# Optimization experiments

Hardware: AMD Instinct MI355X
Metric: run time of the kernel (lower is better)

Reference implementation:

```python
import jax, jax.numpy as jnp
import numpy as np

NUM_TOKENS = 14
DIM = 128
B, N = 8, 128
NUM_ROUNDS = 5


def setup_inputs() -> dict:
    key = jax.random.key(0)
    ks = jax.random.split(key, 10)
    s = 1.0 / np.sqrt(DIM)
    return {
        "tok": jax.random.randint(ks[0], (B, N), 0, NUM_TOKENS),
        "A": jax.random.uniform(ks[1], (B, N, N), dtype=jnp.float32),
        "embed": jax.random.normal(ks[2], (NUM_TOKENS, DIM), dtype=jnp.float32),
        "W1": jax.random.normal(ks[3], (DIM, 2 * DIM), dtype=jnp.float32) * s,
        "b1": jax.random.normal(ks[4], (DIM,), dtype=jnp.float32) * s,
        "W2": jax.random.normal(ks[5], (DIM, DIM), dtype=jnp.float32) * s,
        "b2": jax.random.normal(ks[6], (DIM,), dtype=jnp.float32) * s,
        "Wo1": jax.random.normal(ks[7], (DIM, DIM), dtype=jnp.float32) * s,
        "bo1": jax.random.normal(ks[8], (DIM,), dtype=jnp.float32) * s,
        "Wo2": jax.random.normal(ks[9], (10, DIM), dtype=jnp.float32) * s,
    }


def reference(tok, A, embed, W1, b1, W2, b2, Wo1, bo1, Wo2):
    # Dropout is identity (eval mode / inference reference).
    x = embed[tok]  # [B, N, D]
    d = x.shape[-1]
    # fc1 on concat(x_i, x_j) decomposes into two per-node projections:
    # fc1([x_i, x_j]) = x_i @ W1a^T + x_j @ W1b^T + b1
    W1a, W1b = W1[:, :d], W1[:, d:]
    A_t = jnp.swapaxes(A, 1, 2)  # A.transpose(1, 2)
    for _ in range(NUM_ROUNDS):
        hi = jnp.einsum("bnd,ed->bne", x, W1a)
        hj = jnp.einsum("bnd,ed->bne", x, W1b)
        # pairwise edge MLP: [B, N, N, D]
        h = jax.nn.relu(hi[:, :, None, :] + hj[:, None, :, :] + b1)
        m = jax.nn.relu(jnp.einsum("bijd,ed->bije", h, W2) + b2)
        # mask by transposed adjacency and sum over neighbors j (axis 2)
        msg = jnp.einsum("bij,bije->bie", A_t, m)
        x = x + msg
    def head(z):
        return jax.nn.relu(z @ Wo1.T + bo1) @ Wo2.T
    out = head(x[:, 0, :])                       # [B, 10]
    x_all = head(x.reshape(-1, d)).reshape(x.shape[0], x.shape[1], 10)
    return (out, x_all)
```

## Files before the change

kernel.cpp:

```cpp
#include <hip/hip_runtime.h>
#include <hip/hip_bf16.h>

#define NN 128
#define DD 128

typedef __attribute__((ext_vector_type(8))) short bf16x8;
typedef __attribute__((ext_vector_type(4))) float floatx4;
typedef __attribute__((ext_vector_type(2))) float floatx2;

__device__ __forceinline__ unsigned short f2bf(float f) {
    unsigned int bits = __float_as_uint(f);
    unsigned int r = bits + 0x7FFFu + ((bits >> 16) & 1u);
    return (unsigned short)(r >> 16);
}

__device__ __forceinline__ unsigned short f2bf_hw(float f) {
    unsigned int r;
    asm("v_cvt_pk_bf16_f32 %0, %1, %2" : "=v"(r) : "v"(f), "v"(f));
    return (unsigned short)r;
}

__device__ __forceinline__ unsigned int f2bf_pk(float lo, float hi) {
    unsigned int r;
    asm("v_cvt_pk_bf16_f32 %0, %1, %2" : "=v"(r) : "v"(lo), "v"(hi));
    return r;
}

#define WS_HJB0 0
#define WS_HJB1 65536
#define WS_W1T  131072
#define WS_W2B  148480
#define WS_TABA 157184
#define WS_TABB 158976
#define WS_CNT  159872

__global__ __launch_bounds__(256) void k_init(const int* __restrict__ tok,
                                              const float* __restrict__ embf,
                                              const float* __restrict__ W1f,
                                              const float* __restrict__ b1f,
                                              const float* __restrict__ W2f,
                                              float* __restrict__ ws) {
    unsigned short* gw1t = (unsigned short*)(ws + WS_W1T);
    unsigned short* gw2b = (unsigned short*)(ws + WS_W2B);
    float* taba = ws + WS_TABA;
    unsigned int* tabb32 = (unsigned int*)(ws + WS_TABB);
    int* cnt = (int*)(ws + WS_CNT);
    int blk = blockIdx.x, t = threadIdx.x;

    if (blk == 0) {
        __shared__ __align__(16) unsigned short wt[256 * 136];
        __shared__ __align__(16) unsigned short et_[16 * 136];
        __shared__ float b1s[128];
        for (int idx = t; idx < 256 * 136; idx += 256) {
            int e = idx / 136, d = idx - e * 136;
            wt[idx] = (d < 128) ? f2bf(W1f[(e & 127) * 256 + (e >> 7) * 128 + d])
                                : (unsigned short)0;
        }
        for (int i = t; i < 16 * 136; i += 256) et_[i] = 0;
        if (t < 128) b1s[t] = b1f[t];
        __syncthreads();
        if (t < 224) {
            int v = t >> 4, d0 = (t & 15) * 8;
#pragma unroll
            for (int k2 = 0; k2 < 8; ++k2) et_[v * 136 + d0 + k2] = f2bf(embf[v * 128 + d0 + k2]);
        }
        __syncthreads();
        int wv = t >> 6, lane = t & 63, col = lane & 15, quad = lane >> 4;
        bf16x8 af[4];
#pragma unroll
        for (int ks = 0; ks < 4; ++ks)
            af[ks] = *reinterpret_cast<const bf16x8*>(&et_[col * 136 + ks * 32 + quad * 8]);
#pragma unroll
        for (int c = 0; c < 4; ++c) {
            int nt = wv * 4 + c;
            floatx4 acc = (floatx4){0.f, 0.f, 0.f, 0.f};
#pragma unroll
            for (int ks = 0; ks < 4; ++ks)
                acc = __builtin_amdgcn_mfma_f32_16x16x32_bf16(af[ks],
                        *reinterpret_cast<const bf16x8*>(&wt[(nt * 16 + col) * 136 + ks * 32 + quad * 8]),
                        acc, 0, 0, 0);
            if (nt < 8) {
#pragma unroll
                for (int rr = 0; rr < 4; ++rr) {
                    int v = quad * 4 + rr;
                    if (v < 14) taba[v * 128 + nt * 16 + col] = acc[rr];
                }
            } else {
                int d = (nt - 8) * 16 + col;
                float bv = b1s[d];
#pragma unroll
                for (int rr = 0; rr < 4; ++rr) {
                    float val = acc[rr] + bv;
                    float po = __shfl_xor(val, 1, 64);
                    int v = quad * 4 + rr;
                    if (!(col & 1) && v < 14)
                        tabb32[v * 64 + (d >> 1)] =
                            (unsigned int)f2bf(val) | ((unsigned int)f2bf(po) << 16);
                }
            }
        }
    } else if (blk < 10) {
        int base = (blk - 1) * 4096;
#pragma unroll
        for (int it = 0; it < 16; ++it) {
            int idx = base + it * 256 + t;
            if (idx < 256 * 136) {
                int e = idx / 136, d = idx - e * 136;
                gw1t[idx] = (d < 128) ? f2bf(W1f[(e & 127) * 256 + (e >> 7) * 128 + d])
                                      : (unsigned short)0;
            }
        }
    } else if (blk < 15) {
        int base = (blk - 10) * 4096;
#pragma unroll
        for (int it = 0; it < 16; ++it) {
            int idx = base + it * 256 + t;
            if (idx < 128 * 136) {
                int e = idx / 136, d = idx - e * 136;
                gw2b[idx] = (d < 128) ? f2bf(W2f[e * 128 + d]) : (unsigned short)0;
            }
        }
    } else {
#pragma unroll
        for (int it = 0; it < 4; ++it) cnt[it * 256 + t] = 0;
    }
}

__global__ __launch_bounds__(512, 2) void k_main(const int* __restrict__ tokp,
                                                 const float* __restrict__ embf,
                                                 const float* __restrict__ Af,
                                                 const float* __restrict__ b1f,
                                                 const float* __restrict__ b2f,
                                                 const float* __restrict__ Wo1f,
                                                 const float* __restrict__ bo1f,
                                                 const float* __restrict__ Wo2f,
                                                 float* __restrict__ ws,
                                                 float* __restrict__ outp) {
    __shared__ __align__(16) unsigned short w1t[256 * 136];
    __shared__ __align__(16) unsigned short w2b[128 * 136];
    __shared__ __align__(16) unsigned short xo[4 * 136];
    __shared__ __align__(16) float red[4][4][128];
    __shared__ __align__(16) float zs[4][128];
    __shared__ float a_s[4][128];
    __shared__ __align__(16) float hja_s[4][128];

    const unsigned short* gw1t = (const unsigned short*)(ws + WS_W1T);
    const unsigned short* gw2b = (const unsigned short*)(ws + WS_W2B);
    const float* taba = ws + WS_TABA;
    const unsigned short* tabb16 = (const unsigned short*)(ws + WS_TABB);
    int* cnt = (int*)(ws + WS_CNT);

    int blk = blockIdx.x;
    int b = blk & 7, g = blk >> 3, i0 = g * 4;
    int t = threadIdx.x;
    int wave = t >> 6, lane = t & 63;
    int col = lane & 15, quad = lane >> 4;

    {
        const uint4* s1 = (const uint4*)gw1t; uint4* d1 = (uint4*)w1t;
#pragma unroll
        for (int it = 0; it < 9; ++it) { int idx = it * 512 + t; if (idx < 4352) d1[idx] = s1[idx]; }
        const uint4* s2 = (const uint4*)gw2b; uint4* d2 = (uint4*)w2b;
#pragma unroll
        for (int it = 0; it < 5; ++it) { int idx = it * 512 + t; if (idx < 2176) d2[idx] = s2[idx]; }
    }
    int we = wave & 1, wj = wave >> 1;
    int ebase = we * 64, jbase = wj * 32;
    float b1r0 = 0.f, b1r1 = 0.f;
    if (wave >= 4) {
        b1r0 = b1f[((wave - 4) * 2 + 0) * 16 + col];
        b1r1 = b1f[((wave - 4) * 2 + 1) * 16 + col];
    }
    float b2r[4];
#pragma unroll
    for (int et = 0; et < 4; ++et) b2r[et] = b2f[ebase + et * 16 + col];
    a_s[t >> 7][t & 127] = Af[(b * NN + (t & 127)) * NN + i0 + (t >> 7)];

    int ii_own = t >> 7, e_own = t & 127;
    int trow = tokp[b * NN + i0 + ii_own];
    float xown = embf[trow * DD + e_own];
    hja_s[ii_own][e_own] = taba[trow * 128 + e_own];
    __syncthreads();

    for (int r = 0; r < 5; ++r) {
        unsigned short* gbw = (unsigned short*)(ws + ((r & 1) ? WS_HJB1 : WS_HJB0));

        if (r > 0) {
            bf16x8 af[4];
#pragma unroll
            for (int ks = 0; ks < 4; ++ks) {
                bf16x8 z = {0, 0, 0, 0, 0, 0, 0, 0};
                af[ks] = (col < 4) ? *reinterpret_cast<const bf16x8*>(&xo[col * 136 + ks * 32 + quad * 8]) : z;
            }
            floatx4 acc[2];
            acc[0] = (floatx4){0.f, 0.f, 0.f, 0.f};
            acc[1] = (floatx4){0.f, 0.f, 0.f, 0.f};
#pragma unroll
            for (int u = 0; u < 2; ++u)
#pragma unroll
                for (int ks = 0; ks < 4; ++ks) {
                    int nt = wave * 2 + u;
                    acc[u] = __builtin_amdgcn_mfma_f32_16x16x32_bf16(af[ks],
                        *reinterpret_cast<const bf16x8*>(&w1t[(nt * 16 + col) * 136 + ks * 32 + quad * 8]),
                        acc[u], 0, 0, 0);
                }
            if (wave < 4) {
                if (quad == 0) {
#pragma unroll
                    for (int u = 0; u < 2; ++u)
#pragma unroll
                        for (int rr = 0; rr < 4; ++rr)
                            hja_s[rr][(wave * 2 + u) * 16 + col] = acc[u][rr];
                }
            } else {
#pragma unroll
                for (int u = 0; u < 2; ++u) {
                    float bv = u ? b1r1 : b1r0;
                    int d = ((wave - 4) * 2 + u) * 16 + col;
#pragma unroll
                    for (int rr = 0; rr < 4; ++rr) {
                        float val = acc[u][rr] + bv;
                        float po = __shfl_xor(val, 1, 64);
                        if (quad == 0 && !(col & 1)) {
                            int row = b * NN + i0 + rr;
                            __hip_atomic_store((unsigned int*)gbw + row * 64 + (d >> 1),
                                               f2bf_pk(val, po),
                                               __ATOMIC_RELAXED, __HIP_MEMORY_SCOPE_AGENT);
                        }
                    }
                }
            }
            __atomic_signal_fence(__ATOMIC_SEQ_CST);
            __builtin_amdgcn_s_waitcnt(0);
            __syncthreads();
            if (t == 0) {
                int* myc = cnt + (b * 4 + (r - 1)) * 32;
                __hip_atomic_fetch_add(myc, 1, __ATOMIC_RELAXED, __HIP_MEMORY_SCOPE_AGENT);
                while (__hip_atomic_load(myc, __ATOMIC_RELAXED, __HIP_MEMORY_SCOPE_AGENT) < 32)
                    __builtin_amdgcn_s_sleep(1);
            }
            __syncthreads();
        }

        union U4 { bf16x8 v; unsigned int u[4]; };
        U4 L[2][4];
        {
            const unsigned short* base0;
            const unsigned short* base1;
            if (r == 0) {
                base0 = tabb16 + (size_t)tokp[b * NN + jbase + col] * 128;
                base1 = tabb16 + (size_t)tokp[b * NN + jbase + 16 + col] * 128;
            } else {
                base0 = gbw + (size_t)(b * NN + jbase + col) * 128;
                base1 = gbw + (size_t)(b * NN + jbase + 16 + col) * 128;
            }
            base0 += quad * 8; base1 += quad * 8;
            asm volatile(
                "global_load_dwordx4 %0, %8, off sc0 sc1\n\t"
                "global_load_dwordx4 %1, %8, off offset:64 sc0 sc1\n\t"
                "global_load_dwordx4 %2, %8, off offset:128 sc0 sc1\n\t"
                "global_load_dwordx4 %3, %8, off offset:192 sc0 sc1\n\t"
                "global_load_dwordx4 %4, %9, off sc0 sc1\n\t"
                "global_load_dwordx4 %5, %9, off offset:64 sc0 sc1\n\t"
                "global_load_dwordx4 %6, %9, off offset:128 sc0 sc1\n\t"
                "global_load_dwordx4 %7, %9, off offset:192 sc0 sc1"
                : "=&v"(L[0][0].v), "=&v"(L[0][1].v), "=&v"(L[0][2].v), "=&v"(L[0][3].v),
                  "=&v"(L[1][0].v), "=&v"(L[1][1].v), "=&v"(L[1][2].v), "=&v"(L[1][3].v)
                : "v"(base0), "v"(base1)
                : "memory");
        }
        bf16x8 bw[4][4];
#pragma unroll
        for (int et = 0; et < 4; ++et)
#pragma unroll
            for (int ks = 0; ks < 4; ++ks)
                bw[et][ks] = *reinterpret_cast<const bf16x8*>(&w2b[(ebase + et * 16 + col) * 136 + ks * 32 + quad * 8]);
        asm volatile("s_waitcnt vmcnt(0)" ::: "memory");
        __builtin_amdgcn_sched_barrier(0);

        floatx2 hjc[2][4][4];
#pragma unroll
        for (int jt = 0; jt < 2; ++jt)
#pragma unroll
            for (int ks = 0; ks < 4; ++ks)
#pragma unroll
                for (int p = 0; p < 4; ++p) {
                    floatx2 h2;
                    h2.x = __uint_as_float(L[jt][ks].u[p] << 16);
                    h2.y = __uint_as_float(L[jt][ks].u[p] & 0xFFFF0000u);
                    hjc[jt][ks][p] = h2;
                }

#pragma unroll
        for (int ii = 0; ii < 4; ++ii) {
            floatx4 acc2[2][4];
#pragma unroll
            for (int jt = 0; jt < 2; ++jt)
#pragma unroll
                for (int et = 0; et < 4; ++et) acc2[jt][et] = (floatx4){0.f, 0.f, 0.f, 0.f};
#pragma unroll
            for (int ks = 0; ks < 4; ++ks) {
                int k0 = ks * 32 + quad * 8;
                floatx2 ha[4];
#pragma unroll
                for (int p = 0; p < 4; ++p)
                    ha[p] = *reinterpret_cast<const floatx2*>(&hja_s[ii][k0 + 2 * p]);
#pragma unroll
                for (int jt = 0; jt < 2; ++jt) {
                    U4 Ho;
#pragma unroll
                    for (int p = 0; p < 4; ++p) {
                        floatx2 s2;
                        asm("v_pk_add_f32 %0, %1, %2" : "=v"(s2) : "v"(hjc[jt][ks][p]), "v"(ha[p]));
                        float f0 = fmaxf(s2.x, 0.f);
                        float f1 = fmaxf(s2.y, 0.f);
                        Ho.u[p] = f2bf_pk(f0, f1);
                    }
#pragma unroll
                    for (int et = 0; et < 4; ++et)
                        acc2[jt][et] = __builtin_amdgcn_mfma_f32_16x16x32_bf16(Ho.v, bw[et][ks], acc2[jt][et], 0, 0, 0);
                }
            }
#pragma unroll
            for (int et = 0; et < 4; ++et) {
                float be = b2r[et];
                float s = 0.f;
#pragma unroll
                for (int jt = 0; jt < 2; ++jt) {
                    int j0 = jbase + jt * 16 + quad * 4;
#pragma unroll
                    for (int rr = 0; rr < 4; ++rr)
                        s += a_s[ii][j0 + rr] * fmaxf(acc2[jt][et][rr] + be, 0.f);
                }
                s += __shfl_xor(s, 16, 64);
                s += __shfl_xor(s, 32, 64);
                if (quad == 0) red[wj][ii][ebase + et * 16 + col] = s;
            }
        }
        __syncthreads();
        {
            float msg = red[0][ii_own][e_own] + red[1][ii_own][e_own]
                      + red[2][ii_own][e_own] + red[3][ii_own][e_own];
            xown += msg;
            if (r < 4) xo[ii_own * 136 + e_own] = f2bf_hw(xown);
            else       zs[ii_own][e_own] = xown;
        }
        if (r < 4) __syncthreads();
    }

    float* wo1s = (float*)w1t;
#pragma unroll
    for (int it = 0; it < 8; ++it) {
        int idx4 = it * 512 + t;
        int e = idx4 >> 5, d4 = idx4 & 31;
        float4 wv = reinterpret_cast<const float4*>(Wo1f)[idx4];
        *reinterpret_cast<float4*>(&wo1s[e * 136 + d4 * 4]) = wv;
    }
    __syncthreads();
    {
        int e = t & 127, ii = t >> 7;
        float acc = 0.f;
#pragma unroll
        for (int d4 = 0; d4 < 32; ++d4) {
            float4 w = *reinterpret_cast<const float4*>(&wo1s[e * 136 + d4 * 4]);
            float4 z = *reinterpret_cast<const float4*>(&zs[ii][d4 * 4]);
            acc += w.x * z.x + w.y * z.y + w.z * z.z + w.w * z.w;
        }
        ((float*)red)[ii * 128 + e] = fmaxf(acc + bo1f[e], 0.f);
    }
    __syncthreads();
    if (t < 40) {
        int ii = t / 10, o = t - ii * 10;
        const float* rsrow = (const float*)red + ii * 128;
        const float4* w2r = reinterpret_cast<const float4*>(Wo2f + o * DD);
        float s = 0.f;
#pragma unroll
        for (int e4 = 0; e4 < 32; ++e4) {
            float4 rv = *reinterpret_cast<const float4*>(&rsrow[e4 * 4]);
            float4 wv = w2r[e4];
            s += rv.x * wv.x + rv.y * wv.y + rv.z * wv.z + rv.w * wv.w;
        }
        int row = b * NN + i0 + ii;
        outp[80 + row * 10 + o] = s;
        if (i0 + ii == 0) outp[b * 10 + o] = s;
    }
}

extern "C" void kernel_launch(void* const* d_in, const int* in_sizes, int n_in,
                              void* d_out, int out_size, void* d_ws, size_t ws_size,
                              hipStream_t stream) {
    const int*   tok  = (const int*)d_in[0];
    const float* Af   = (const float*)d_in[1];
    const float* embf = (const float*)d_in[2];
    const float* W1f  = (const float*)d_in[3];
    const float* b1f  = (const float*)d_in[4];
    const float* W2f  = (const float*)d_in[5];
    const float* b2f  = (const float*)d_in[6];
    const float* Wo1f = (const float*)d_in[7];
    const float* bo1f = (const float*)d_in[8];
    const float* Wo2f = (const float*)d_in[9];

    float* ws  = (float*)d_ws;
    float* out = (float*)d_out;

    k_init<<<16, 256, 0, stream>>>(tok, embf, W1f, b1f, W2f, ws);
    k_main<<<256, 512, 0, stream>>>(tok, embf, Af, b1f, b2f, Wo1f, bo1f, Wo2f, ws, out);
}
```

Baseline: 172.2 us.

## Double block size to 1024 threads, stream W1 from global, drop round-zero lookup tables

The main kernel now runs 16 waves per block, and each wave handles 16 neighbor rows instead of 32, which halves per-wave register state. W1 is no longer staged into shared memory. Each wave instead reads its own W1 fragment from global memory every round, freeing LDS for the Wo1 buffer and a larger reduction array. The precomputed embedding-projection tables in the init kernel are removed, so round zero computes hi/hj through the same path as the other rounds. That adds one more cross-block barrier round, plus repeated global reads of W1 fragments.

```diff
diff --git a/kernel.cpp b/kernel.cpp
--- a/kernel.cpp
+++ b/kernel.cpp
@@ -30,77 +30,17 @@
 #define WS_HJB1 65536
 #define WS_W1T  131072
 #define WS_W2B  148480
-#define WS_TABA 157184
-#define WS_TABB 158976
-#define WS_CNT  159872
-
-__global__ __launch_bounds__(256) void k_init(const int* __restrict__ tok,
-                                              const float* __restrict__ embf,
-                                              const float* __restrict__ W1f,
-                                              const float* __restrict__ b1f,
+#define WS_CNT  157184
+
+__global__ __launch_bounds__(256) void k_init(const float* __restrict__ W1f,
                                               const float* __restrict__ W2f,
                                               float* __restrict__ ws) {
     unsigned short* gw1t = (unsigned short*)(ws + WS_W1T);
     unsigned short* gw2b = (unsigned short*)(ws + WS_W2B);
-    float* taba = ws + WS_TABA;
-    unsigned int* tabb32 = (unsigned int*)(ws + WS_TABB);
     int* cnt = (int*)(ws + WS_CNT);
     int blk = blockIdx.x, t = threadIdx.x;
-
-    if (blk == 0) {
-        __shared__ __align__(16) unsigned short wt[256 * 136];
-        __shared__ __align__(16) unsigned short et_[16 * 136];
-        __shared__ float b1s[128];
-        for (int idx = t; idx < 256 * 136; idx += 256) {
-            int e = idx / 136, d = idx - e * 136;
-            wt[idx] = (d < 128) ? f2bf(W1f[(e & 127) * 256 + (e >> 7) * 128 + d])
-                                : (unsigned short)0;
-        }
-        for (int i = t; i < 16 * 136; i += 256) et_[i] = 0;
-        if (t < 128) b1s[t] = b1f[t];
-        __syncthreads();
-        if (t < 224) {
-            int v = t >> 4, d0 = (t & 15) * 8;
-#pragma unroll
-            for (int k2 = 0; k2 < 8; ++k2) et_[v * 136 + d0 + k2] = f2bf(embf[v * 128 + d0 + k2]);
-        }
-        __syncthreads();
-        int wv = t >> 6, lane = t & 63, col = lane & 15, quad = lane >> 4;
-        bf16x8 af[4];
-#pragma unroll
-        for (int ks = 0; ks < 4; ++ks)
-            af[ks] = *reinterpret_cast<const bf16x8*>(&et_[col * 136 + ks * 32 + quad * 8]);
-#pragma unroll
-        for (int c = 0; c < 4; ++c) {
-            int nt = wv * 4 + c;
-            floatx4 acc = (floatx4){0.f, 0.f, 0.f, 0.f};
-#pragma unroll
-            for (int ks = 0; ks < 4; ++ks)
-                acc = __builtin_amdgcn_mfma_f32_16x16x32_bf16(af[ks],
-                        *reinterpret_cast<const bf16x8*>(&wt[(nt * 16 + col) * 136 + ks * 32 + quad * 8]),
-                        acc, 0, 0, 0);
-            if (nt < 8) {
-#pragma unroll
-                for (int rr = 0; rr < 4; ++rr) {
-                    int v = quad * 4 + rr;
-                    if (v < 14) taba[v * 128 + nt * 16 + col] = acc[rr];
-                }
-            } else {
-                int d = (nt - 8) * 16 + col;
-                float bv = b1s[d];
-#pragma unroll
-                for (int rr = 0; rr < 4; ++rr) {
-                    float val = acc[rr] + bv;
-                    float po = __shfl_xor(val, 1, 64);
-                    int v = quad * 4 + rr;
-                    if (!(col & 1) && v < 14)
-                        tabb32[v * 64 + (d >> 1)] =
-                            (unsigned int)f2bf(val) | ((unsigned int)f2bf(po) << 16);
-                }
-            }
-        }
-    } else if (blk < 10) {
-        int base = (blk - 1) * 4096;
+    if (blk < 9) {
+        int base = blk * 4096;
 #pragma unroll
         for (int it = 0; it < 16; ++it) {
             int idx = base + it * 256 + t;
@@ -110,8 +50,8 @@
                                       : (unsigned short)0;
             }
         }
-    } else if (blk < 15) {
-        int base = (blk - 10) * 4096;
+    } else if (blk < 14) {
+        int base = (blk - 9) * 4096;
 #pragma unroll
         for (int it = 0; it < 16; ++it) {
             int idx = base + it * 256 + t;
@@ -122,32 +62,30 @@
         }
     } else {
 #pragma unroll
-        for (int it = 0; it < 4; ++it) cnt[it * 256 + t] = 0;
-    }
-}
-
-__global__ __launch_bounds__(512, 2) void k_main(const int* __restrict__ tokp,
-                                                 const float* __restrict__ embf,
-                                                 const float* __restrict__ Af,
-                                                 const float* __restrict__ b1f,
-                                                 const float* __restrict__ b2f,
-                                                 const float* __restrict__ Wo1f,
-                                                 const float* __restrict__ bo1f,
-                                                 const float* __restrict__ Wo2f,
-                                                 float* __restrict__ ws,
-                                                 float* __restrict__ outp) {
-    __shared__ __align__(16) unsigned short w1t[256 * 136];
+        for (int it = 0; it < 5; ++it) cnt[it * 256 + t] = 0;
+    }
+}
+
+__global__ __launch_bounds__(1024, 4) void k_main(const int* __restrict__ tokp,
+                                                  const float* __restrict__ embf,
+                                                  const float* __restrict__ Af,
+                                                  const float* __restrict__ b1f,
+                                                  const float* __restrict__ b2f,
+                                                  const float* __restrict__ Wo1f,
+                                                  const float* __restrict__ bo1f,
+                                                  const float* __restrict__ Wo2f,
+                                                  float* __restrict__ ws,
+                                                  float* __restrict__ outp) {
     __shared__ __align__(16) unsigned short w2b[128 * 136];
     __shared__ __align__(16) unsigned short xo[4 * 136];
-    __shared__ __align__(16) float red[4][4][128];
+    __shared__ __align__(16) float red[8][4][128];
     __shared__ __align__(16) float zs[4][128];
     __shared__ float a_s[4][128];
     __shared__ __align__(16) float hja_s[4][128];
+    __shared__ __align__(16) float wo1s[128 * 136];
 
     const unsigned short* gw1t = (const unsigned short*)(ws + WS_W1T);
     const unsigned short* gw2b = (const unsigned short*)(ws + WS_W2B);
-    const float* taba = ws + WS_TABA;
-    const unsigned short* tabb16 = (const unsigned short*)(ws + WS_TABB);
     int* cnt = (int*)(ws + WS_CNT);
 
     int blk = blockIdx.x;
@@ -157,116 +95,86 @@
     int col = lane & 15, quad = lane >> 4;
 
     {
-        const uint4* s1 = (const uint4*)gw1t; uint4* d1 = (uint4*)w1t;
-#pragma unroll
-        for (int it = 0; it < 9; ++it) { int idx = it * 512 + t; if (idx < 4352) d1[idx] = s1[idx]; }
         const uint4* s2 = (const uint4*)gw2b; uint4* d2 = (uint4*)w2b;
 #pragma unroll
-        for (int it = 0; it < 5; ++it) { int idx = it * 512 + t; if (idx < 2176) d2[idx] = s2[idx]; }
-    }
+        for (int it = 0; it < 3; ++it) { int idx = it * 1024 + t; if (idx < 2176) d2[idx] = s2[idx]; }
+    }
+    float b1r = (wave >= 8) ? b1f[(wave - 8) * 16 + col] : 0.f;
     int we = wave & 1, wj = wave >> 1;
-    int ebase = we * 64, jbase = wj * 32;
-    float b1r0 = 0.f, b1r1 = 0.f;
-    if (wave >= 4) {
-        b1r0 = b1f[((wave - 4) * 2 + 0) * 16 + col];
-        b1r1 = b1f[((wave - 4) * 2 + 1) * 16 + col];
-    }
+    int ebase = we * 64, jbase = wj * 16;
     float b2r[4];
 #pragma unroll
     for (int et = 0; et < 4; ++et) b2r[et] = b2f[ebase + et * 16 + col];
-    a_s[t >> 7][t & 127] = Af[(b * NN + (t & 127)) * NN + i0 + (t >> 7)];
-
-    int ii_own = t >> 7, e_own = t & 127;
+
+    int ii_own = (t >> 7) & 3, e_own = t & 127, half = t >> 9;
+    if (half == 0) a_s[ii_own][e_own] = Af[(b * NN + e_own) * NN + i0 + ii_own];
     int trow = tokp[b * NN + i0 + ii_own];
     float xown = embf[trow * DD + e_own];
-    hja_s[ii_own][e_own] = taba[trow * 128 + e_own];
+    if (half == 0) xo[ii_own * 136 + e_own] = f2bf_hw(xown);
     __syncthreads();
+
+    const unsigned short* w1row = gw1t + (wave * 16 + col) * 136 + quad * 8;
 
     for (int r = 0; r < 5; ++r) {
         unsigned short* gbw = (unsigned short*)(ws + ((r & 1) ? WS_HJB1 : WS_HJB0));
 
-        if (r > 0) {
+        {
+            bf16x8 w1f[4];
+#pragma unroll
+            for (int ks = 0; ks < 4; ++ks)
+                w1f[ks] = *reinterpret_cast<const bf16x8*>(w1row + ks * 32);
             bf16x8 af[4];
 #pragma unroll
             for (int ks = 0; ks < 4; ++ks) {
                 bf16x8 z = {0, 0, 0, 0, 0, 0, 0, 0};
                 af[ks] = (col < 4) ? *reinterpret_cast<const bf16x8*>(&xo[col * 136 + ks * 32 + quad * 8]) : z;
             }
-            floatx4 acc[2];
-            acc[0] = (floatx4){0.f, 0.f, 0.f, 0.f};
-            acc[1] = (floatx4){0.f, 0.f, 0.f, 0.f};
-#pragma unroll
-            for (int u = 0; u < 2; ++u)
-#pragma unroll
-                for (int ks = 0; ks < 4; ++ks) {
-                    int nt = wave * 2 + u;
-                    acc[u] = __builtin_amdgcn_mfma_f32_16x16x32_bf16(af[ks],
-                        *reinterpret_cast<const bf16x8*>(&w1t[(nt * 16 + col) * 136 + ks * 32 + quad * 8]),
-                        acc[u], 0, 0, 0);
-                }
-            if (wave < 4) {
+            floatx4 acc = (floatx4){0.f, 0.f, 0.f, 0.f};
+#pragma unroll
+            for (int ks = 0; ks < 4; ++ks)
+                acc = __builtin_amdgcn_mfma_f32_16x16x32_bf16(af[ks], w1f[ks], acc, 0, 0, 0);
+            if (wave < 8) {
                 if (quad == 0) {
 #pragma unroll
-                    for (int u = 0; u < 2; ++u)
-#pragma unroll
-                        for (int rr = 0; rr < 4; ++rr)
-                            hja_s[rr][(wave * 2 + u) * 16 + col] = acc[u][rr];
+                    for (int rr = 0; rr < 4; ++rr) hja_s[rr][wave * 16 + col] = acc[rr];
                 }
             } else {
-#pragma unroll
-                for (int u = 0; u < 2; ++u) {
-                    float bv = u ? b1r1 : b1r0;
-                    int d = ((wave - 4) * 2 + u) * 16 + col;
-#pragma unroll
-                    for (int rr = 0; rr < 4; ++rr) {
-                        float val = acc[u][rr] + bv;
-                        float po = __shfl_xor(val, 1, 64);
-                        if (quad == 0 && !(col & 1)) {
-                            int row = b * NN + i0 + rr;
-                            __hip_atomic_store((unsigned int*)gbw + row * 64 + (d >> 1),
-                                               f2bf_pk(val, po),
-                                               __ATOMIC_RELAXED, __HIP_MEMORY_SCOPE_AGENT);
-                        }
+                int d = (wave - 8) * 16 + col;
+#pragma unroll
+                for (int rr = 0; rr < 4; ++rr) {
+                    float val = acc[rr] + b1r;
+                    float po = __shfl_xor(val, 1, 64);
+                    if (quad == 0 && !(col & 1)) {
+                        int row = b * NN + i0 + rr;
+                        __hip_atomic_store((unsigned int*)gbw + row * 64 + (d >> 1),
+                                           f2bf_pk(val, po),
+                                           __ATOMIC_RELAXED, __HIP_MEMORY_SCOPE_AGENT);
                     }
                 }
             }
-            __atomic_signal_fence(__ATOMIC_SEQ_CST);
-            __builtin_amdgcn_s_waitcnt(0);
-            __syncthreads();
-            if (t == 0) {
-                int* myc = cnt + (b * 4 + (r - 1)) * 32;
-                __hip_atomic_fetch_add(myc, 1, __ATOMIC_RELAXED, __HIP_MEMORY_SCOPE_AGENT);
-                while (__hip_atomic_load(myc, __ATOMIC_RELAXED, __HIP_MEMORY_SCOPE_AGENT) < 32)
-                    __builtin_amdgcn_s_sleep(1);
-            }
-            __syncthreads();
-        }
+        }
+        __atomic_signal_fence(__ATOMIC_SEQ_CST);
+        __builtin_amdgcn_s_waitcnt(0);
+        __syncthreads();
+        if (t == 0) {
+            int* myc = cnt + (b * 5 + r) * 32;
+            __hip_atomic_fetch_add(myc, 1, __ATOMIC_RELAXED, __HIP_MEMORY_SCOPE_AGENT);
+            while (__hip_atomic_load(myc, __ATOMIC_RELAXED, __HIP_MEMORY_SCOPE_AGENT) < 32)
+                __builtin_amdgcn_s_sleep(1);
+        }
+        __syncthreads();
 
         union U4 { bf16x8 v; unsigned int u[4]; };
-        U4 L[2][4];
+        U4 L[4];
         {
-            const unsigned short* base0;
-            const unsigned short* base1;
-            if (r == 0) {
-                base0 = tabb16 + (size_t)tokp[b * NN + jbase + col] * 128;
-                base1 = tabb16 + (size_t)tokp[b * NN + jbase + 16 + col] * 128;
-            } else {
-                base0 = gbw + (size_t)(b * NN + jbase + col) * 128;
-                base1 = gbw + (size_t)(b * NN + jbase + 16 + col) * 128;
-            }
-            base0 += quad * 8; base1 += quad * 8;
+            const unsigned short* base0 = gbw + (size_t)(b * NN + jbase + col) * 128 + quad * 8;
             asm volatile(
-                "global_load_dwordx4 %0, %8, off sc0 sc1\n\t"
-                "global_load_dwordx4 %1, %8, off offset:64 sc0 sc1\n\t"
-                "global_load_dwordx4 %2, %8, off offset:128 sc0 sc1\n\t"
-                "global_load_dwordx4 %3, %8, off offset:192 sc0 sc1\n\t"
-                "global_load_dwordx4 %4, %9, off sc0 sc1\n\t"
-                "global_load_dwordx4 %5, %9, off offset:64 sc0 sc1\n\t"
-                "global_load_dwordx4 %6, %9, off offset:128 sc0 sc1\n\t"
-                "global_load_dwordx4 %7, %9, off offset:192 sc0 sc1"
-                : "=&v"(L[0][0].v), "=&v"(L[0][1].v), "=&v"(L[0][2].v), "=&v"(L[0][3].v),
-                  "=&v"(L[1][0].v), "=&v"(L[1][1].v), "=&v"(L[1][2].v), "=&v"(L[1][3].v)
-                : "v"(base0), "v"(base1)
+                "global_load_dwordx4 %0, %4, off sc0 sc1\n\t"
+                "global_load_dwordx4 %1, %4, off offset:64 sc0 sc1\n\t"
+                "global_load_dwordx4 %2, %4, off offset:128 sc0 sc1\n\t"
+                "global_load_dwordx4 %3, %4, off offset:192 sc0 sc1"
+                : "=&v"(L[0].v), "=&v"(L[1].v), "=&v"(L[2].v), "=&v"(L[3].v)
+                : "v"(base0)
                 : "memory");
         }
         bf16x8 bw[4][4];
@@ -278,26 +186,25 @@
         asm volatile("s_waitcnt vmcnt(0)" ::: "memory");
         __builtin_amdgcn_sched_barrier(0);
 
-        floatx2 hjc[2][4][4];
-#pragma unroll
-        for (int jt = 0; jt < 2; ++jt)
-#pragma unroll
-            for (int ks = 0; ks < 4; ++ks)
-#pragma unroll
-                for (int p = 0; p < 4; ++p) {
-                    floatx2 h2;
-                    h2.x = __uint_as_float(L[jt][ks].u[p] << 16);
-                    h2.y = __uint_as_float(L[jt][ks].u[p] & 0xFFFF0000u);
-                    hjc[jt][ks][p] = h2;
-                }
+        floatx2 hjc[4][4];
+#pragma unroll
+        for (int ks = 0; ks < 4; ++ks)
+#pragma unroll
+            for (int p = 0; p < 4; ++p) {
+                floatx2 h2;
+                h2.x = __uint_as_float(L[ks].u[p] << 16);
+                h2.y = __uint_as_float(L[ks].u[p] & 0xFFFF0000u);
+                hjc[ks][p] = h2;
+            }
 
 #pragma unroll
         for (int ii = 0; ii < 4; ++ii) {
-            floatx4 acc2[2][4];
-#pragma unroll
-            for (int jt = 0; jt < 2; ++jt)
-#pragma unroll
-                for (int et = 0; et < 4; ++et) acc2[jt][et] = (floatx4){0.f, 0.f, 0.f, 0.f};
+            floatx4 acc2[4];
+#pragma unroll
+            for (int et = 0; et < 4; ++et) acc2[et] = (floatx4){0.f, 0.f, 0.f, 0.f};
+            float ar[4];
+#pragma unroll
+            for (int rr = 0; rr < 4; ++rr) ar[rr] = a_s[ii][jbase + quad * 4 + rr];
 #pragma unroll
             for (int ks = 0; ks < 4; ++ks) {
                 int k0 = ks * 32 + quad * 8;
@@ -305,42 +212,36 @@
 #pragma unroll
                 for (int p = 0; p < 4; ++p)
                     ha[p] = *reinterpret_cast<const floatx2*>(&hja_s[ii][k0 + 2 * p]);
-#pragma unroll
-                for (int jt = 0; jt < 2; ++jt) {
-                    U4 Ho;
-#pragma unroll
-                    for (int p = 0; p < 4; ++p) {
-                        floatx2 s2;
-                        asm("v_pk_add_f32 %0, %1, %2" : "=v"(s2) : "v"(hjc[jt][ks][p]), "v"(ha[p]));
-                        float f0 = fmaxf(s2.x, 0.f);
-                        float f1 = fmaxf(s2.y, 0.f);
-                        Ho.u[p] = f2bf_pk(f0, f1);
-                    }
-#pragma unroll
-                    for (int et = 0; et < 4; ++et)
-                        acc2[jt][et] = __builtin_amdgcn_mfma_f32_16x16x32_bf16(Ho.v, bw[et][ks], acc2[jt][et], 0, 0, 0);
+                U4 Ho;
+#pragma unroll
+                for (int p = 0; p < 4; ++p) {
+                    floatx2 s2;
+                    asm("v_pk_add_f32 %0, %1, %2" : "=v"(s2) : "v"(hjc[ks][p]), "v"(ha[p]));
+                    float f0 = fmaxf(s2.x, 0.f);
+                    float f1 = fmaxf(s2.y, 0.f);
+                    Ho.u[p] = f2bf_pk(f0, f1);
                 }
+#pragma unroll
+                for (int et = 0; et < 4; ++et)
+                    acc2[et] = __builtin_amdgcn_mfma_f32_16x16x32_bf16(Ho.v, bw[et][ks], acc2[et], 0, 0, 0);
             }
 #pragma unroll
             for (int et = 0; et < 4; ++et) {
                 float be = b2r[et];
                 float s = 0.f;
 #pragma unroll
-                for (int jt = 0; jt < 2; ++jt) {
-                    int j0 = jbase + jt * 16 + quad * 4;
-#pragma unroll
-                    for (int rr = 0; rr < 4; ++rr)
-                        s += a_s[ii][j0 + rr] * fmaxf(acc2[jt][et][rr] + be, 0.f);
-                }
+                for (int rr = 0; rr < 4; ++rr)
+                    s += ar[rr] * fmaxf(acc2[et][rr] + be, 0.f);
                 s += __shfl_xor(s, 16, 64);
                 s += __shfl_xor(s, 32, 64);
                 if (quad == 0) red[wj][ii][ebase + et * 16 + col] = s;
             }
         }
         __syncthreads();
-        {
-            float msg = red[0][ii_own][e_own] + red[1][ii_own][e_own]
-                      + red[2][ii_own][e_own] + red[3][ii_own][e_own];
+        if (half == 0) {
+            float msg = 0.f;
+#pragma unroll
+            for (int w8 = 0; w8 < 8; ++w8) msg += red[w8][ii_own][e_own];
             xown += msg;
             if (r < 4) xo[ii_own * 136 + e_own] = f2bf_hw(xown);
             else       zs[ii_own][e_own] = xown;
@@ -348,17 +249,16 @@
         if (r < 4) __syncthreads();
     }
 
-    float* wo1s = (float*)w1t;
-#pragma unroll
-    for (int it = 0; it < 8; ++it) {
-        int idx4 = it * 512 + t;
+#pragma unroll
+    for (int it = 0; it < 4; ++it) {
+        int idx4 = it * 1024 + t;
         int e = idx4 >> 5, d4 = idx4 & 31;
         float4 wv = reinterpret_cast<const float4*>(Wo1f)[idx4];
         *reinterpret_cast<float4*>(&wo1s[e * 136 + d4 * 4]) = wv;
     }
     __syncthreads();
-    {
-        int e = t & 127, ii = t >> 7;
+    if (t < 512) {
+        int ii = t >> 7, e = t & 127;
         float acc = 0.f;
 #pragma unroll
         for (int d4 = 0; d4 < 32; ++d4) {
@@ -403,6 +303,6 @@
     float* ws  = (float*)d_ws;
     float* out = (float*)d_out;
 
-    k_init<<<16, 256, 0, stream>>>(tok, embf, W1f, b1f, W2f, ws);
-    k_main<<<256, 512, 0, stream>>>(tok, embf, Af, b1f, b2f, Wo1f, bo1f, Wo2f, ws, out);
-}
+    k_init<<<15, 256, 0, stream>>>(W1f, W2f, ws);
+    k_main<<<256, 1024, 0, stream>>>(tok, embf, Af, b1f, b2f, Wo1f, bo1f, Wo2f, ws, out);
+}
```

After: 213.7 us. 24.1% more time.
